# Kernel tuning notes

Measured on AMD Instinct MI355X. Metric: run time of the kernel, lower is better.

The kernel has to match this reference:

```python
import jax, jax.numpy as jnp
import numpy as np

B, T, E, H = 2, 2048, 1024, 16
D = E // H          # head_size = 64
DF = 4 * E          # FFN inner dim


def setup_inputs() -> dict:
    key = jax.random.key(0)
    ks = jax.random.split(key, 10)
    s = E ** -0.5
    return {
        "x":  jax.random.normal(ks[0], (B, T, E), jnp.float32),
        "Wq": jax.random.normal(ks[1], (H, E, D), jnp.float32) * s,
        "Wk": jax.random.normal(ks[2], (H, E, D), jnp.float32) * s,
        "Wv": jax.random.normal(ks[3], (H, E, D), jnp.float32) * s,
        "Wo": jax.random.normal(ks[4], (E, E), jnp.float32) * s,
        "bo": jnp.zeros((E,), jnp.float32),
        "W1": jax.random.normal(ks[5], (E, DF), jnp.float32) * s,
        "b1": jnp.zeros((DF,), jnp.float32),
        "W2": jax.random.normal(ks[6], (DF, E), jnp.float32) * (DF ** -0.5),
        "b2": jnp.zeros((E,), jnp.float32),
    }


def reference(x, Wq, Wk, Wv, Wo, bo, W1, b1, W2, b2):
    Bx, Tx, C = x.shape
    # NOTE: source scales by C**-0.5 where C = n_embed (not head_size) -- faithful.
    scale = C ** -0.5
    q = jnp.einsum('btc,hcd->bhtd', x, Wq)
    k = jnp.einsum('btc,hcd->bhtd', x, Wk)
    v = jnp.einsum('btc,hcd->bhtd', x, Wv)
    scores = jnp.einsum('bhtd,bhsd->bhts', q, k) * scale   # [B,H,T,T]
    causal = jnp.tril(jnp.ones((Tx, Tx), bool))
    scores = jnp.where(causal, scores, -jnp.inf)
    attn = jax.nn.softmax(scores, axis=-1)
    out = jnp.einsum('bhts,bhsd->bhtd', attn, v)
    out = out.transpose(0, 2, 1, 3).reshape(Bx, Tx, C)     # concat heads
    x = x + (out @ Wo + bo)                                # residual + projection
    h = jax.nn.relu(x @ W1 + b1)
    x = x + (h @ W2 + b2)                                  # residual + FFN
    return x
```

## Files before the change

kernel.cpp:

```cpp
#include <hip/hip_runtime.h>

#define B_ 2
#define T_ 2048
#define E_ 1024
#define H_ 16
#define D_ 64
#define DF_ 4096
#define M_ (B_*T_)
#define NQKV_ 3072

typedef unsigned short u16;
typedef __attribute__((ext_vector_type(8))) short short8;
typedef __attribute__((ext_vector_type(4))) float f32x4;
typedef __attribute__((ext_vector_type(16))) float f32x16;

__device__ __forceinline__ u16 f2bf(float f) {
  unsigned u = __builtin_bit_cast(unsigned, f);
  u += 0x7FFFu + ((u >> 16) & 1u);
  return (u16)(u >> 16);
}
__device__ __forceinline__ unsigned pack2bf(float a, float b) {
  return (unsigned)f2bf(a) | ((unsigned)f2bf(b) << 16);
}
__device__ __forceinline__ unsigned cvtpk(float a, float b) {
  unsigned r;
  asm("v_cvt_pk_bf16_f32 %0, %1, %2" : "=v"(r) : "v"(a), "v"(b));
  return r;
}
__device__ __forceinline__ float bf2f(u16 u) {
  return __builtin_bit_cast(float, (unsigned)u << 16);
}
__device__ __forceinline__ float vmax16(const f32x16& v) {
  float a0 = fmaxf(v[0], v[1]),   a1 = fmaxf(v[2], v[3]);
  float a2 = fmaxf(v[4], v[5]),   a3 = fmaxf(v[6], v[7]);
  float a4 = fmaxf(v[8], v[9]),   a5 = fmaxf(v[10], v[11]);
  float a6 = fmaxf(v[12], v[13]), a7 = fmaxf(v[14], v[15]);
  float b0 = fmaxf(a0, a1), b1 = fmaxf(a2, a3), b2 = fmaxf(a4, a5), b3 = fmaxf(a6, a7);
  return fmaxf(fmaxf(b0, b1), fmaxf(b2, b3));
}
__device__ __forceinline__ float vsum16(const f32x16& v) {
  float a0 = v[0] + v[1],   a1 = v[2] + v[3];
  float a2 = v[4] + v[5],   a3 = v[6] + v[7];
  float a4 = v[8] + v[9],   a5 = v[10] + v[11];
  float a6 = v[12] + v[13], a7 = v[14] + v[15];
  float b0 = a0 + a1, b1 = a2 + a3, b2 = a4 + a5, b3 = a6 + a7;
  return (b0 + b1) + (b2 + b3);
}

__device__ __forceinline__ void gload_lds16(const u16* g, u16* l) {
  __builtin_amdgcn_global_load_lds((const __attribute__((address_space(1))) void*)g,
                                   (__attribute__((address_space(3))) void*)l, 16, 0, 0);
}

__global__ __launch_bounds__(256) void cast_bf16_kernel(const float* __restrict__ in,
                                                        u16* __restrict__ out, int n4) {
  int i = blockIdx.x * 256 + threadIdx.x;
  if (i >= n4) return;
  float4 v = ((const float4*)in)[i];
  uint2 r;
  r.x = (unsigned)f2bf(v.x) | ((unsigned)f2bf(v.y) << 16);
  r.y = (unsigned)f2bf(v.z) | ((unsigned)f2bf(v.w) << 16);
  ((uint2*)out)[i] = r;
}

__global__ __launch_bounds__(256) void transpose_cast_kernel(const float* __restrict__ in,
                                                             u16* __restrict__ out,
                                                             int R, int C, int outld) {
  __shared__ float tile[32][33];
  int z = blockIdx.z;
  int c0 = blockIdx.x * 32, r0 = blockIdx.y * 32;
  int tx = threadIdx.x & 31, ty = threadIdx.x >> 5;
  const float* ip = in + (size_t)z * R * C;
#pragma unroll
  for (int i = 0; i < 32; i += 8)
    tile[ty + i][tx] = ip[(size_t)(r0 + ty + i) * C + (c0 + tx)];
  __syncthreads();
#pragma unroll
  for (int i = 0; i < 32; i += 8)
    out[(size_t)(z * C + c0 + ty + i) * outld + (r0 + tx)] = f2bf(tile[tx][ty + i]);
}

__global__ __launch_bounds__(256) void transpose_u16_kernel(const u16* __restrict__ in,
                                                            u16* __restrict__ out,
                                                            int R, int C, int ldin) {
  __shared__ __attribute__((aligned(16))) u16 tile[64][72];
  int c0 = blockIdx.x * 64, r0 = blockIdx.y * 64;
  int t = threadIdx.x;
  int tr = t >> 4, tc = (t & 15) * 4;
#pragma unroll
  for (int i = 0; i < 4; i++)
    *(uint2*)&tile[tr + i * 16][tc] = *(const uint2*)&in[(size_t)(r0 + tr + i * 16) * ldin + c0 + tc];
  __syncthreads();
  int rr = (t & 15) * 4, cc0 = t >> 4;
#pragma unroll
  for (int i = 0; i < 4; i++) {
    int cc = cc0 + i * 16;
    u16 a = tile[rr][cc], b = tile[rr + 1][cc], c = tile[rr + 2][cc], d = tile[rr + 3][cc];
    uint2 v;
    v.x = (unsigned)a | ((unsigned)b << 16);
    v.y = (unsigned)c | ((unsigned)d << 16);
    *(uint2*)&out[(size_t)(c0 + cc) * R + r0 + rr] = v;
  }
}

template<int TM, int TN, bool BIAS, bool RELU, bool RES, bool OF32, bool OBF>
__global__ __launch_bounds__(256, 2)
void gemm_bt(const u16* __restrict__ A,
             const u16* __restrict__ Bt,
             int M, int N, int K, int lda, int ldb,
             const float* __restrict__ bias,
             const float* __restrict__ res,
             float* __restrict__ outf,
             u16* __restrict__ outb) {
  constexpr int MF = TM / 32;
  constexpr int NF = TN / 32;
  constexpr int ACH = TM / 32;
  constexpr int BCH = TN / 32;
  __shared__ __attribute__((aligned(16))) u16 As[2][TM][64];
  __shared__ __attribute__((aligned(16))) u16 Bs[2][TN][64];
  int m0 = blockIdx.y * TM, n0 = blockIdx.x * TN;
  int z = blockIdx.z;
  A  += (size_t)z * K;
  Bt += (size_t)z * K;
  if (OF32 && outf) outf += (size_t)z * M * N;
  if (OBF && outb)  outb += (size_t)z * M * N;
  int tid = threadIdx.x;
  int lane = tid & 63, w = tid >> 6;
  int wr = w >> 1, wc = w & 1;
  int lg = lane >> 4, lq = lane & 15;
  int srow8 = lane >> 3;
  int scolsw = ((lane & 7) ^ srow8) * 8;

  const u16* aSrcP[ACH];
  const u16* bSrcP[BCH];
#pragma unroll
  for (int j = 0; j < ACH; j++)
    aSrcP[j] = &A[(size_t)(m0 + w * (ACH * 8) + j * 8 + srow8) * lda + scolsw];
#pragma unroll
  for (int j = 0; j < BCH; j++)
    bSrcP[j] = &Bt[(size_t)(n0 + w * (BCH * 8) + j * 8 + srow8) * ldb + scolsw];

  auto stage = [&](int buf, int k0) {
#pragma unroll
    for (int j = 0; j < ACH; j++)
      gload_lds16(aSrcP[j] + k0, &As[buf][w * (ACH * 8) + j * 8][0]);
#pragma unroll
    for (int j = 0; j < BCH; j++)
      gload_lds16(bSrcP[j] + k0, &Bs[buf][w * (BCH * 8) + j * 8][0]);
  };

  f32x4 acc[MF][NF] = {};
  int lqx = lq & 7;

  stage(0, 0);
  __syncthreads();
  int cur = 0;
  for (int k0 = 0; k0 < K; k0 += 64) {
    if (k0 + 64 < K) stage(cur ^ 1, k0 + 64);
#pragma unroll
    for (int kk = 0; kk < 2; kk++) {
      short8 af[MF], bf[NF];
      int csw = ((lg + kk * 4) ^ lqx) * 8;
#pragma unroll
      for (int m = 0; m < MF; m++) af[m] = *(const short8*)&As[cur][wr * (TM / 2) + m * 16 + lq][csw];
#pragma unroll
      for (int n = 0; n < NF; n++) bf[n] = *(const short8*)&Bs[cur][wc * (TN / 2) + n * 16 + lq][csw];
#pragma unroll
      for (int m = 0; m < MF; m++)
#pragma unroll
        for (int n = 0; n < NF; n++)
          acc[m][n] = __builtin_amdgcn_mfma_f32_16x16x32_bf16(af[m], bf[n], acc[m][n], 0, 0, 0);
    }
    __syncthreads();
    cur ^= 1;
  }

#pragma unroll
  for (int m = 0; m < MF; m++)
#pragma unroll
    for (int n = 0; n < NF; n++) {
      int row = m0 + wr * (TM / 2) + m * 16 + lg * 4;
      int col = n0 + wc * (TN / 2) + n * 16 + lq;
      float bv = BIAS ? bias[col] : 0.f;
      float vv[4];
#pragma unroll
      for (int r = 0; r < 4; r++) {
        float v = acc[m][n][r];
        if (BIAS) v += bv;
        if (RES)  v += res[(size_t)(row + r) * N + col];
        if (RELU) v = fmaxf(v, 0.f);
        if (OF32) outf[(size_t)(row + r) * N + col] = v;
        vv[r] = v;
      }
      if (OBF) {
        unsigned p01 = cvtpk(vv[0], vv[1]);
        unsigned p23 = cvtpk(vv[2], vv[3]);
        outb[(size_t)(row + 0) * N + col] = (u16)p01;
        outb[(size_t)(row + 1) * N + col] = (u16)(p01 >> 16);
        outb[(size_t)(row + 2) * N + col] = (u16)p23;
        outb[(size_t)(row + 3) * N + col] = (u16)(p23 >> 16);
      }
    }
}

__global__ __launch_bounds__(256) void reduce2_kernel(const float* __restrict__ x1,
                                                      const u16* __restrict__ p0,
                                                      const u16* __restrict__ p1,
                                                      const float* __restrict__ b2,
                                                      float* __restrict__ out) {
  int i = blockIdx.x * 256 + threadIdx.x;
  float4 xv = ((const float4*)x1)[i];
  ushort4 a = ((const ushort4*)p0)[i];
  ushort4 b = ((const ushort4*)p1)[i];
  const float4 bb = *(const float4*)&b2[(i * 4) & (E_ - 1)];
  float4 r;
  r.x = xv.x + bf2f(a.x) + bf2f(b.x) + bb.x;
  r.y = xv.y + bf2f(a.y) + bf2f(b.y) + bb.y;
  r.z = xv.z + bf2f(a.z) + bf2f(b.z) + bb.z;
  r.w = xv.w + bf2f(a.w) + bf2f(b.w) + bb.w;
  ((float4*)out)[i] = r;
}

__global__ __launch_bounds__(256) void attn_kernel(const u16* __restrict__ qkv,
                                                   const u16* __restrict__ Vt,
                                                   u16* __restrict__ attn) {
  __shared__ __attribute__((aligned(16))) u16 Ks[64 * 64];
  __shared__ __attribute__((aligned(16))) u16 Vs[64 * 64];
  int bid = blockIdx.x;
  int pp = bid >> 8, rrb = bid & 255;
  int h  = rrb >> 4;
  int jj = rrb & 15;
  int b  = pp;
  int qt = pp ? (15 - jj) : jj;
  int tid = threadIdx.x;
  int lane = tid & 63, w = tid >> 6;
  int l31 = lane & 31, hh = lane >> 5;
  int q0w = qt * 128 + w * 32;
  int q_abs = q0w + l31;

  short8 qf[4];
  const u16* Qrow = qkv + (size_t)(b * T_ + q_abs) * NQKV_ + h * 64;
#pragma unroll
  for (int ks = 0; ks < 4; ks++) qf[ks] = *(const short8*)&Qrow[ks * 16 + hh * 8];

  const u16* Kbase  = qkv + (size_t)(b * T_) * NQKV_ + 1024 + h * 64;
  const u16* Vtbase = Vt + (size_t)(h * 64) * M_ + b * T_;

  int r0s = tid >> 3, c0s = tid & 7;
  int r1s = r0s + 32;
  unsigned kd0 = (unsigned)((r0s * 128 + c0s * 16) ^ ((r0s & 7) << 4));
  unsigned kd1 = (unsigned)((r1s * 128 + c0s * 16) ^ ((r1s & 7) << 4));
  const u16* Kg0 = &Kbase[(size_t)r0s * NQKV_ + c0s * 8];
  const u16* Kg1 = &Kbase[(size_t)r1s * NQKV_ + c0s * 8];
  const u16* Vg0 = &Vtbase[(size_t)r0s * M_ + c0s * 8];
  const u16* Vg1 = &Vtbase[(size_t)r1s * M_ + c0s * 8];

  f32x16 o[2] = {};
  float m_run = -__builtin_inff(), l_run = 0.f;
  const float SCL = 0.03125f;
  const int s_stop = qt * 128 + 128;

  uint4 kr0 = *(const uint4*)Kg0;
  uint4 kr1 = *(const uint4*)Kg1;
  uint4 vr0 = *(const uint4*)Vg0;
  uint4 vr1 = *(const uint4*)Vg1;

  for (int s0 = 0; s0 < s_stop; s0 += 64) {
    __syncthreads();
    *(uint4*)((char*)Ks + kd0) = kr0;
    *(uint4*)((char*)Ks + kd1) = kr1;
    *(uint4*)((char*)Vs + kd0) = vr0;
    *(uint4*)((char*)Vs + kd1) = vr1;
    if (s0 + 64 < s_stop) {
      kr0 = *(const uint4*)&Kg0[(size_t)(s0 + 64) * NQKV_];
      kr1 = *(const uint4*)&Kg1[(size_t)(s0 + 64) * NQKV_];
      vr0 = *(const uint4*)&Vg0[s0 + 64];
      vr1 = *(const uint4*)&Vg1[s0 + 64];
    }
    __syncthreads();
    if (s0 > q0w + 31) continue;

    f32x16 st[2];
    __builtin_amdgcn_s_setprio(1);
#pragma unroll
    for (int c = 0; c < 2; c++) {
      f32x16 acc = {};
      int key = c * 32 + l31;
#pragma unroll
      for (int ks = 0; ks < 4; ks++) {
        unsigned off = (unsigned)((key * 128 + ks * 32 + hh * 16) ^ ((key & 7) << 4));
        short8 kf = *(const short8*)((const char*)Ks + off);
        acc = __builtin_amdgcn_mfma_f32_32x32x16_bf16(kf, qf[ks], acc, 0, 0, 0);
      }
      st[c] = acc;
    }
    __builtin_amdgcn_s_setprio(0);

    if (s0 + 63 > q0w) {
#pragma unroll
      for (int c = 0; c < 2; c++)
#pragma unroll
        for (int r = 0; r < 16; r++) {
          int key = s0 + c * 32 + (r & 3) + 8 * (r >> 2) + 4 * hh;
          st[c][r] = (key > q_abs) ? -__builtin_inff() : st[c][r];
        }
    }
    float tmax = fmaxf(vmax16(st[0]), vmax16(st[1]));
    tmax = fmaxf(tmax, __shfl_xor(tmax, 32));

    if (!__all(tmax - m_run <= 256.0f)) {
      float newm = fmaxf(m_run, tmax);
      float fac = __expf((m_run - newm) * SCL);
      l_run *= fac;
      o[0] *= fac;
      o[1] *= fac;
      m_run = newm;
    }
    float nm = -m_run * SCL;
#pragma unroll
    for (int c = 0; c < 2; c++)
#pragma unroll
      for (int r = 0; r < 16; r++)
        st[c][r] = __expf(fmaf(st[c][r], SCL, nm));
    float psum = vsum16(st[0]) + vsum16(st[1]);
    psum += __shfl_xor(psum, 32);
    l_run += psum;

    unsigned wds[2][8];
#pragma unroll
    for (int c = 0; c < 2; c++)
#pragma unroll
      for (int i = 0; i < 8; i++)
        wds[c][i] = cvtpk(st[c][2 * i], st[c][2 * i + 1]);

    __builtin_amdgcn_s_setprio(1);
#pragma unroll
    for (int ks16 = 0; ks16 < 4; ks16++) {
      int c = ks16 >> 1, e = ks16 & 1;
      unsigned send0 = hh ? wds[c][4 * e]     : wds[c][4 * e + 2];
      unsigned send1 = hh ? wds[c][4 * e + 1] : wds[c][4 * e + 3];
      unsigned recv0 = (unsigned)__shfl_xor((int)send0, 32);
      unsigned recv1 = (unsigned)__shfl_xor((int)send1, 32);
      uint4 fw;
      fw.x = hh ? recv0 : wds[c][4 * e];
      fw.y = hh ? recv1 : wds[c][4 * e + 1];
      fw.z = hh ? wds[c][4 * e + 2] : recv0;
      fw.w = hh ? wds[c][4 * e + 3] : recv1;
      short8 pf = __builtin_bit_cast(short8, fw);
#pragma unroll
      for (int dc = 0; dc < 2; dc++) {
        int d = dc * 32 + l31;
        unsigned off = (unsigned)((d * 128 + ks16 * 32 + hh * 16) ^ ((d & 7) << 4));
        short8 vf = *(const short8*)((const char*)Vs + off);
        o[dc] = __builtin_amdgcn_mfma_f32_32x32x16_bf16(vf, pf, o[dc], 0, 0, 0);
      }
    }
    __builtin_amdgcn_s_setprio(0);
  }

  float inv = 1.f / l_run;
  const size_t orow = (size_t)(b * T_ + q_abs) * E_ + h * 64;
#pragma unroll
  for (int dc = 0; dc < 2; dc++)
#pragma unroll
    for (int a = 0; a < 4; a++) {
      float e0 = o[dc][4 * a] * inv,     e1 = o[dc][4 * a + 1] * inv;
      float e2 = o[dc][4 * a + 2] * inv, e3 = o[dc][4 * a + 3] * inv;
      uint2 r;
      r.x = cvtpk(e0, e1);
      r.y = cvtpk(e2, e3);
      *(uint2*)&attn[orow + dc * 32 + 8 * a + 4 * hh] = r;
    }
}

extern "C" void kernel_launch(void* const* d_in, const int* in_sizes, int n_in,
                              void* d_out, int out_size, void* d_ws, size_t ws_size,
                              hipStream_t stream) {
  const float* x  = (const float*)d_in[0];
  const float* Wq = (const float*)d_in[1];
  const float* Wk = (const float*)d_in[2];
  const float* Wv = (const float*)d_in[3];
  const float* Wo = (const float*)d_in[4];
  const float* bo = (const float*)d_in[5];
  const float* W1 = (const float*)d_in[6];
  const float* b1 = (const float*)d_in[7];
  const float* W2 = (const float*)d_in[8];
  const float* b2 = (const float*)d_in[9];
  float* out = (float*)d_out;

  const size_t MB = 1048576;
  char* ws = (char*)d_ws;
  u16* xb    = (u16*)(ws + 0);
  u16* WqkvT = (u16*)(ws + 8 * MB);
  u16* WoT   = (u16*)(ws + 14 * MB);
  u16* W1T   = (u16*)(ws + 16 * MB);
  u16* W2T   = (u16*)(ws + 24 * MB);
  u16* qkv   = (u16*)(ws + 32 * MB);
  u16* attn  = (u16*)(ws + 56 * MB);
  float* x1  = (float*)(ws + 64 * MB);
  u16* Vtb   = (u16*)(ws + 64 * MB);
  u16* x1b   = (u16*)(ws + 0);
  u16* hbuf  = (u16*)(ws + 32 * MB);
  u16* pbuf  = (u16*)(ws + 0);

  cast_bf16_kernel<<<(M_ * E_ / 4 + 255) / 256, 256, 0, stream>>>(x, xb, M_ * E_ / 4);
  transpose_cast_kernel<<<dim3(2, 32, 16),  256, 0, stream>>>(Wq, WqkvT,                E_, D_, E_);
  transpose_cast_kernel<<<dim3(2, 32, 16),  256, 0, stream>>>(Wk, WqkvT + 1024 * 1024,  E_, D_, E_);
  transpose_cast_kernel<<<dim3(2, 32, 16),  256, 0, stream>>>(Wv, WqkvT + 2048 * 1024,  E_, D_, E_);
  transpose_cast_kernel<<<dim3(32, 32, 1),  256, 0, stream>>>(Wo, WoT, E_, E_, E_);
  transpose_cast_kernel<<<dim3(128, 32, 1), 256, 0, stream>>>(W1, W1T, E_, DF_, E_);
  transpose_cast_kernel<<<dim3(32, 128, 1), 256, 0, stream>>>(W2, W2T, DF_, E_, DF_);

  gemm_bt<128,128,false,false,false,false,true><<<dim3(NQKV_ / 128, M_ / 128), 256, 0, stream>>>(
      xb, WqkvT, M_, NQKV_, E_, E_, E_, nullptr, nullptr, nullptr, qkv);

  transpose_u16_kernel<<<dim3(E_ / 64, M_ / 64), 256, 0, stream>>>(qkv + 2048, Vtb, M_, E_, NQKV_);

  attn_kernel<<<B_ * H_ * (T_ / 128), 256, 0, stream>>>(qkv, Vtb, attn);

  gemm_bt<64,128,true,false,true,true,true><<<dim3(E_ / 128, M_ / 64), 256, 0, stream>>>(
      attn, WoT, M_, E_, E_, E_, E_, bo, x, x1, x1b);
  gemm_bt<128,128,true,true,false,false,true><<<dim3(DF_ / 128, M_ / 128), 256, 0, stream>>>(
      x1b, W1T, M_, DF_, E_, E_, E_, b1, nullptr, nullptr, hbuf);
  gemm_bt<128,128,false,false,false,false,true><<<dim3(E_ / 128, M_ / 128, 2), 256, 0, stream>>>(
      hbuf, W2T, M_, E_, DF_ / 2, DF_, DF_, nullptr, nullptr, nullptr, pbuf);
  reduce2_kernel<<<M_ * E_ / 4 / 256, 256, 0, stream>>>(x1, pbuf, pbuf + (size_t)M_ * E_, b2, out);
}
```

Measured before the change: 236.7 us.

## Double-buffer K/V tiles in attention LDS and use packed bf16 convert in cast

The attention kernel now keeps two LDS buffers for K and V. The next tile is written into the spare buffer while the current one is consumed, so each iteration needs one barrier instead of two. The bf16 cast kernel also switches from manual rounding to the packed hardware convert instruction. The cost is doubled LDS use per block (32KB), which may lower occupancy. The initial prefetch assumes at least two tiles exist, which holds because s_stop is at least 128.

```diff
diff --git a/kernel.cpp b/kernel.cpp
--- a/kernel.cpp
+++ b/kernel.cpp
@@ -19,9 +19,6 @@
   u += 0x7FFFu + ((u >> 16) & 1u);
   return (u16)(u >> 16);
 }
-__device__ __forceinline__ unsigned pack2bf(float a, float b) {
-  return (unsigned)f2bf(a) | ((unsigned)f2bf(b) << 16);
-}
 __device__ __forceinline__ unsigned cvtpk(float a, float b) {
   unsigned r;
   asm("v_cvt_pk_bf16_f32 %0, %1, %2" : "=v"(r) : "v"(a), "v"(b));
@@ -58,8 +55,8 @@
   if (i >= n4) return;
   float4 v = ((const float4*)in)[i];
   uint2 r;
-  r.x = (unsigned)f2bf(v.x) | ((unsigned)f2bf(v.y) << 16);
-  r.y = (unsigned)f2bf(v.z) | ((unsigned)f2bf(v.w) << 16);
+  r.x = cvtpk(v.x, v.y);
+  r.y = cvtpk(v.z, v.w);
   ((uint2*)out)[i] = r;
 }
 
@@ -224,8 +221,8 @@
 __global__ __launch_bounds__(256) void attn_kernel(const u16* __restrict__ qkv,
                                                    const u16* __restrict__ Vt,
                                                    u16* __restrict__ attn) {
-  __shared__ __attribute__((aligned(16))) u16 Ks[64 * 64];
-  __shared__ __attribute__((aligned(16))) u16 Vs[64 * 64];
+  __shared__ __attribute__((aligned(16))) u16 Ks[2][64 * 64];
+  __shared__ __attribute__((aligned(16))) u16 Vs[2][64 * 64];
   int bid = blockIdx.x;
   int pp = bid >> 8, rrb = bid & 255;
   int h  = rrb >> 4;
@@ -264,98 +261,117 @@
   uint4 kr1 = *(const uint4*)Kg1;
   uint4 vr0 = *(const uint4*)Vg0;
   uint4 vr1 = *(const uint4*)Vg1;
+  *(uint4*)((char*)&Ks[0][0] + kd0) = kr0;
+  *(uint4*)((char*)&Ks[0][0] + kd1) = kr1;
+  *(uint4*)((char*)&Vs[0][0] + kd0) = vr0;
+  *(uint4*)((char*)&Vs[0][0] + kd1) = vr1;
+  kr0 = *(const uint4*)&Kg0[(size_t)64 * NQKV_];
+  kr1 = *(const uint4*)&Kg1[(size_t)64 * NQKV_];
+  vr0 = *(const uint4*)&Vg0[64];
+  vr1 = *(const uint4*)&Vg1[64];
+  __syncthreads();
+  int cur = 0;
 
   for (int s0 = 0; s0 < s_stop; s0 += 64) {
+    if (s0 + 64 < s_stop) {
+      char* kb = (char*)&Ks[cur ^ 1][0];
+      char* vb = (char*)&Vs[cur ^ 1][0];
+      *(uint4*)(kb + kd0) = kr0;
+      *(uint4*)(kb + kd1) = kr1;
+      *(uint4*)(vb + kd0) = vr0;
+      *(uint4*)(vb + kd1) = vr1;
+      if (s0 + 128 < s_stop) {
+        kr0 = *(const uint4*)&Kg0[(size_t)(s0 + 128) * NQKV_];
+        kr1 = *(const uint4*)&Kg1[(size_t)(s0 + 128) * NQKV_];
+        vr0 = *(const uint4*)&Vg0[s0 + 128];
+        vr1 = *(const uint4*)&Vg1[s0 + 128];
+      }
+    }
+
+    if (s0 <= q0w + 31) {
+      const char* KsC = (const char*)&Ks[cur][0];
+      const char* VsC = (const char*)&Vs[cur][0];
+
+      f32x16 st[2];
+      __builtin_amdgcn_s_setprio(1);
+#pragma unroll
+      for (int c = 0; c < 2; c++) {
+        f32x16 acc = {};
+        int key = c * 32 + l31;
+#pragma unroll
+        for (int ks = 0; ks < 4; ks++) {
+          unsigned off = (unsigned)((key * 128 + ks * 32 + hh * 16) ^ ((key & 7) << 4));
+          short8 kf = *(const short8*)(KsC + off);
+          acc = __builtin_amdgcn_mfma_f32_32x32x16_bf16(kf, qf[ks], acc, 0, 0, 0);
+        }
+        st[c] = acc;
+      }
+      __builtin_amdgcn_s_setprio(0);
+
+      if (s0 + 63 > q0w) {
+#pragma unroll
+        for (int c = 0; c < 2; c++)
+#pragma unroll
+          for (int r = 0; r < 16; r++) {
+            int key = s0 + c * 32 + (r & 3) + 8 * (r >> 2) + 4 * hh;
+            st[c][r] = (key > q_abs) ? -__builtin_inff() : st[c][r];
+          }
+      }
+      float tmax = fmaxf(vmax16(st[0]), vmax16(st[1]));
+      tmax = fmaxf(tmax, __shfl_xor(tmax, 32));
+
+      if (!__all(tmax - m_run <= 256.0f)) {
+        float newm = fmaxf(m_run, tmax);
+        float fac = __expf((m_run - newm) * SCL);
+        l_run *= fac;
+        o[0] *= fac;
+        o[1] *= fac;
+        m_run = newm;
+      }
+      float nm = -m_run * SCL;
+#pragma unroll
+      for (int c = 0; c < 2; c++)
+#pragma unroll
+        for (int r = 0; r < 16; r++)
+          st[c][r] = __expf(fmaf(st[c][r], SCL, nm));
+      float psum = vsum16(st[0]) + vsum16(st[1]);
+      psum += __shfl_xor(psum, 32);
+      l_run += psum;
+
+      unsigned wds[2][8];
+#pragma unroll
+      for (int c = 0; c < 2; c++)
+#pragma unroll
+        for (int i = 0; i < 8; i++)
+          wds[c][i] = cvtpk(st[c][2 * i], st[c][2 * i + 1]);
+
+      __builtin_amdgcn_s_setprio(1);
+#pragma unroll
+      for (int ks16 = 0; ks16 < 4; ks16++) {
+        int c = ks16 >> 1, e = ks16 & 1;
+        unsigned send0 = hh ? wds[c][4 * e]     : wds[c][4 * e + 2];
+        unsigned send1 = hh ? wds[c][4 * e + 1] : wds[c][4 * e + 3];
+        unsigned recv0 = (unsigned)__shfl_xor((int)send0, 32);
+        unsigned recv1 = (unsigned)__shfl_xor((int)send1, 32);
+        uint4 fw;
+        fw.x = hh ? recv0 : wds[c][4 * e];
+        fw.y = hh ? recv1 : wds[c][4 * e + 1];
+        fw.z = hh ? wds[c][4 * e + 2] : recv0;
+        fw.w = hh ? wds[c][4 * e + 3] : recv1;
+        short8 pf = __builtin_bit_cast(short8, fw);
+#pragma unroll
+        for (int dc = 0; dc < 2; dc++) {
+          int d = dc * 32 + l31;
+          unsigned off = (unsigned)((d * 128 + ks16 * 32 + hh * 16) ^ ((d & 7) << 4));
+          short8 vf = *(const short8*)(VsC + off);
+          o[dc] = __builtin_amdgcn_mfma_f32_32x32x16_bf16(vf, pf, o[dc], 0, 0, 0);
+        }
+      }
+      __builtin_amdgcn_s_setprio(0);
+    }
+
     __syncthreads();
-    *(uint4*)((char*)Ks + kd0) = kr0;
-    *(uint4*)((char*)Ks + kd1) = kr1;
-    *(uint4*)((char*)Vs + kd0) = vr0;
-    *(uint4*)((char*)Vs + kd1) = vr1;
-    if (s0 + 64 < s_stop) {
-      kr0 = *(const uint4*)&Kg0[(size_t)(s0 + 64) * NQKV_];
-      kr1 = *(const uint4*)&Kg1[(size_t)(s0 + 64) * NQKV_];
-      vr0 = *(const uint4*)&Vg0[s0 + 64];
-      vr1 = *(const uint4*)&Vg1[s0 + 64];
-    }
-    __syncthreads();
-    if (s0 > q0w + 31) continue;
-
-    f32x16 st[2];
-    __builtin_amdgcn_s_setprio(1);
-#pragma unroll
-    for (int c = 0; c < 2; c++) {
-      f32x16 acc = {};
-      int key = c * 32 + l31;
-#pragma unroll
-      for (int ks = 0; ks < 4; ks++) {
-        unsigned off = (unsigned)((key * 128 + ks * 32 + hh * 16) ^ ((key & 7) << 4));
-        short8 kf = *(const short8*)((const char*)Ks + off);
-        acc = __builtin_amdgcn_mfma_f32_32x32x16_bf16(kf, qf[ks], acc, 0, 0, 0);
-      }
-      st[c] = acc;
-    }
-    __builtin_amdgcn_s_setprio(0);
-
-    if (s0 + 63 > q0w) {
-#pragma unroll
-      for (int c = 0; c < 2; c++)
-#pragma unroll
-        for (int r = 0; r < 16; r++) {
-          int key = s0 + c * 32 + (r & 3) + 8 * (r >> 2) + 4 * hh;
-          st[c][r] = (key > q_abs) ? -__builtin_inff() : st[c][r];
-        }
-    }
-    float tmax = fmaxf(vmax16(st[0]), vmax16(st[1]));
-    tmax = fmaxf(tmax, __shfl_xor(tmax, 32));
-
-    if (!__all(tmax - m_run <= 256.0f)) {
-      float newm = fmaxf(m_run, tmax);
-      float fac = __expf((m_run - newm) * SCL);
-      l_run *= fac;
-      o[0] *= fac;
-      o[1] *= fac;
-      m_run = newm;
-    }
-    float nm = -m_run * SCL;
-#pragma unroll
-    for (int c = 0; c < 2; c++)
-#pragma unroll
-      for (int r = 0; r < 16; r++)
-        st[c][r] = __expf(fmaf(st[c][r], SCL, nm));
-    float psum = vsum16(st[0]) + vsum16(st[1]);
-    psum += __shfl_xor(psum, 32);
-    l_run += psum;
-
-    unsigned wds[2][8];
-#pragma unroll
-    for (int c = 0; c < 2; c++)
-#pragma unroll
-      for (int i = 0; i < 8; i++)
-        wds[c][i] = cvtpk(st[c][2 * i], st[c][2 * i + 1]);
-
-    __builtin_amdgcn_s_setprio(1);
-#pragma unroll
-    for (int ks16 = 0; ks16 < 4; ks16++) {
-      int c = ks16 >> 1, e = ks16 & 1;
-      unsigned send0 = hh ? wds[c][4 * e]     : wds[c][4 * e + 2];
-      unsigned send1 = hh ? wds[c][4 * e + 1] : wds[c][4 * e + 3];
-      unsigned recv0 = (unsigned)__shfl_xor((int)send0, 32);
-      unsigned recv1 = (unsigned)__shfl_xor((int)send1, 32);
-      uint4 fw;
-      fw.x = hh ? recv0 : wds[c][4 * e];
-      fw.y = hh ? recv1 : wds[c][4 * e + 1];
-      fw.z = hh ? wds[c][4 * e + 2] : recv0;
-      fw.w = hh ? wds[c][4 * e + 3] : recv1;
-      short8 pf = __builtin_bit_cast(short8, fw);
-#pragma unroll
-      for (int dc = 0; dc < 2; dc++) {
-        int d = dc * 32 + l31;
-        unsigned off = (unsigned)((d * 128 + ks16 * 32 + hh * 16) ^ ((d & 7) << 4));
-        short8 vf = *(const short8*)((const char*)Vs + off);
-        o[dc] = __builtin_amdgcn_mfma_f32_32x32x16_bf16(vf, pf, o[dc], 0, 0, 0);
-      }
-    }
-    __builtin_amdgcn_s_setprio(0);
+    cur ^= 1;
   }
 
   float inv = 1.f / l_run;
```

Measured after the change: 238.6 us. No clear change (+0.8%).
